# Performance work log

Hardware: AMD Instinct MI355X
Metric: run time of the kernel (lower is better)

Reference implementation:

```python
import jax, jax.numpy as jnp
import numpy as np

SIGMA = 0.005  # hard-coded in naive_corres


def _neg_sqdist(x, y):
    # -||x_i - y_j||^2 via GEMM expansion; x:[B,N,D], y:[B,M,D] -> [B,N,M]
    x2 = jnp.sum(x * x, axis=-1)  # [B,N]
    y2 = jnp.sum(y * y, axis=-1)  # [B,M]
    xy = jnp.einsum('bnd,bmd->bnm', x, y)
    return -(x2[:, :, None] + y2[:, None, :] - 2.0 * xy)


def setup_inputs() -> dict:
    key = jax.random.key(0)
    k1, k2, k3, k4 = jax.random.split(key, 4)
    B, N, D = 2, 4096, 32
    points = jax.random.uniform(k1, (B, N, 3), dtype=jnp.float32)
    pointfea1 = jax.random.normal(k2, (B, N, D), dtype=jnp.float32)
    pointfea2 = jax.random.normal(k3, (B, N, D), dtype=jnp.float32)
    weights = jax.random.uniform(k4, (B, N, 1), dtype=jnp.float32) / N
    return {"points": points, "pointfea1": pointfea1,
            "pointfea2": pointfea2, "weights": weights}


def reference(points, pointfea1, pointfea2, weights):
    # --- naive_corres ---
    p = points / SIGMA
    point_dist2 = _neg_sqdist(p, p)                       # [B,N,N]
    point_loggauss = jax.nn.log_softmax(point_dist2, axis=2)
    fea_dist2 = _neg_sqdist(pointfea1, pointfea2)         # [B,N,N]
    fea_logsoftmax = jax.nn.log_softmax(fea_dist2, axis=2)
    # ce per source point, weighted, summed over points -> [B]
    ce = -jnp.sum(jnp.exp(point_loggauss) * fea_logsoftmax, axis=2)  # [B,N]
    ce_loss = jnp.sum(ce * weights[..., 0], axis=1)       # [B]
    # --- reg_loss (pos_is_in_fea=True -> skip first 3 channels) ---
    reg = (pointfea1[:, :, 3:] ** 2 + pointfea2[:, :, 3:] ** 2)
    reg_loss = reg.mean(axis=2).mean(axis=1)              # [B]
    return ce_loss, reg_loss
```

## Files before the change

kernel.cpp:

```cpp
#include <hip/hip_runtime.h>
#include <math.h>


#define NPTS 4096
#define ROWS_TOT 8192
#define DF 32

#define L2E  1.4426950408889634f
#define LN2  0.6931471805599453f
#define FSC  1.6986436f
#define PSC  240.2244f

typedef _Float16 half8 __attribute__((ext_vector_type(8)));
typedef float f4 __attribute__((ext_vector_type(4)));

__global__ void kA_prep(const float* __restrict__ pts,
                        const float* __restrict__ f1g,
                        const float* __restrict__ f2g,
                        float* __restrict__ pp1, float* __restrict__ pp2,
                        _Float16* __restrict__ fragA, _Float16* __restrict__ fragB,
                        float* __restrict__ regp, float* __restrict__ out) {
    const int r = blockIdx.x * 64 + threadIdx.x;
    if (r < 4) out[r] = 0.0f;
    const int jt = r >> 4;
    const int c  = r & 15;

    float n1, n2, reg1, reg2;
    {
        const float4* f2v = (const float4*)(f2g + (size_t)r * DF);
        float vals[32];
        float s = 0.0f;
#pragma unroll
        for (int q = 0; q < 8; ++q) {
            float4 v = f2v[q];
            vals[4*q]=v.x; vals[4*q+1]=v.y; vals[4*q+2]=v.z; vals[4*q+3]=v.w;
            s += v.x*v.x + v.y*v.y + v.z*v.z + v.w*v.w;
        }
        n2 = s;
        reg2 = s - vals[0]*vals[0] - vals[1]*vals[1] - vals[2]*vals[2];
        half8* fv = (half8*)fragB;
#pragma unroll
        for (int kb = 0; kb < 4; ++kb) {
            half8 h;
#pragma unroll
            for (int i = 0; i < 8; ++i) h[i] = (_Float16)(vals[kb*8+i] * FSC);
            fv[(size_t)jt*64 + kb*16 + c] = h;
        }
    }
    {
        const float4* f1v = (const float4*)(f1g + (size_t)r * DF);
        float vals[32];
        float s = 0.0f;
#pragma unroll
        for (int q = 0; q < 8; ++q) {
            float4 v = f1v[q];
            vals[4*q]=v.x; vals[4*q+1]=v.y; vals[4*q+2]=v.z; vals[4*q+3]=v.w;
            s += v.x*v.x + v.y*v.y + v.z*v.z + v.w*v.w;
        }
        n1 = s;
        reg1 = s - vals[0]*vals[0] - vals[1]*vals[1] - vals[2]*vals[2];
        half8* fv = (half8*)fragA;
#pragma unroll
        for (int kb = 0; kb < 4; ++kb) {
            half8 h;
#pragma unroll
            for (int i = 0; i < 8; ++i) h[i] = (_Float16)(vals[kb*8+i] * FSC);
            fv[(size_t)jt*64 + kb*16 + c] = h;
        }
    }
    const float* pp = pts + (size_t)r * 3;
    const float px = pp[0]*PSC, py = pp[1]*PSC, pz = pp[2]*PSC;
    ((float4*)pp1)[r] = make_float4(px, py, pz, n1 * L2E);
    ((float4*)pp2)[r] = make_float4(px, py, pz, n2 * L2E);
    regp[r] = reg1 + reg2;
}

__launch_bounds__(512)
__global__ void kB_main(const float* __restrict__ pp1,
                        const float* __restrict__ pp2,
                        const _Float16* __restrict__ fragA,
                        const _Float16* __restrict__ fragB,
                        float* __restrict__ part) {
    __shared__ float sS[8][32], sT[8][32], sF[8][32];

    const int tid = threadIdx.x;
    const int l = tid & 63, wv = tid >> 6;
    const int ip = blockIdx.x >> 1;
    const int jh = blockIdx.x & 1;
    const int b  = ip >> 7;
    const int i0g = ip * 32;
    const int lr = l & 15, lk = l >> 4;

    const half8 afA = ((const half8*)fragA)[(size_t)(ip * 2)     * 64 + l];
    const half8 afB = ((const half8*)fragA)[(size_t)(ip * 2 + 1) * 64 + l];

    const int rbA = i0g + lk * 4;
    const int rbB = i0g + 16 + lk * 4;
    f4 qxA, qyA, qzA, qwA, qxB, qyB, qzB, qwB;
#pragma unroll
    for (int e = 0; e < 4; ++e) {
        const float4 qA = ((const float4*)pp1)[rbA + e];
        const float4 qB = ((const float4*)pp1)[rbB + e];
        qxA[e] = qA.x; qyA[e] = qA.y; qzA[e] = qA.z; qwA[e] = qA.w;
        qxB[e] = qB.x; qyB[e] = qB.y; qzB[e] = qB.z; qwB[e] = qB.w;
    }

    const int jt0 = b * 256 + jh * 128 + wv * 16;
    const int j0  = b * NPTS + jh * 2048 + wv * 256 + lr;
    const half8*  fbase = (const half8*)fragB + ((size_t)jt0 * 64 + l);
    const float4* pbase = (const float4*)pp2 + j0;

    f4 spA = {0,0,0,0}, tAA = {0,0,0,0}, sfA = {0,0,0,0};
    f4 spB = {0,0,0,0}, tAB = {0,0,0,0}, sfB = {0,0,0,0};
    const f4 zero = {0.f, 0.f, 0.f, 0.f};

    half8  bfC = fbase[0];
    float4 pwC = pbase[0];
#pragma unroll
    for (int t = 0; t < 16; ++t) {
        half8  bfN = bfC;
        float4 pwN = pwC;
        if (t < 15) {
            bfN = fbase[(t + 1) * 64];
            pwN = pbase[(t + 1) * 16];
        }
        const f4 ccA = __builtin_amdgcn_mfma_f32_16x16x32_f16(afA, bfC, zero, 0, 0, 0);
        const f4 ccB = __builtin_amdgcn_mfma_f32_16x16x32_f16(afB, bfC, zero, 0, 0, 0);
        {
            const f4 fd = ccA - qwA - pwC.w;
            const f4 dx = qxA - pwC.x;
            const f4 dy = qyA - pwC.y;
            const f4 dz = qzA - pwC.z;
            const f4 s  = dx*dx + dy*dy + dz*dz;
            f4 ep, ef;
#pragma unroll
            for (int e = 0; e < 4; ++e) {
                ep[e] = __builtin_amdgcn_exp2f(-s[e]);
                ef[e] = __builtin_amdgcn_exp2f(fd[e]);
            }
            spA += ep; tAA += ep * fd; sfA += ef;
        }
        {
            const f4 fd = ccB - qwB - pwC.w;
            const f4 dx = qxB - pwC.x;
            const f4 dy = qyB - pwC.y;
            const f4 dz = qzB - pwC.z;
            const f4 s  = dx*dx + dy*dy + dz*dz;
            f4 ep, ef;
#pragma unroll
            for (int e = 0; e < 4; ++e) {
                ep[e] = __builtin_amdgcn_exp2f(-s[e]);
                ef[e] = __builtin_amdgcn_exp2f(fd[e]);
            }
            spB += ep; tAB += ep * fd; sfB += ef;
        }
        bfC = bfN;
        pwC = pwN;
    }

#pragma unroll
    for (int m = 1; m < 16; m <<= 1) {
#pragma unroll
        for (int e = 0; e < 4; ++e) {
            spA[e] += __shfl_xor(spA[e], m);
            tAA[e] += __shfl_xor(tAA[e], m);
            sfA[e] += __shfl_xor(sfA[e], m);
            spB[e] += __shfl_xor(spB[e], m);
            tAB[e] += __shfl_xor(tAB[e], m);
            sfB[e] += __shfl_xor(sfB[e], m);
        }
    }
    if (lr == 0) {
#pragma unroll
        for (int e = 0; e < 4; ++e) {
            sS[wv][lk * 4 + e]      = spA[e];
            sT[wv][lk * 4 + e]      = tAA[e];
            sF[wv][lk * 4 + e]      = sfA[e];
            sS[wv][16 + lk * 4 + e] = spB[e];
            sT[wv][16 + lk * 4 + e] = tAB[e];
            sF[wv][16 + lk * 4 + e] = sfB[e];
        }
    }
    __syncthreads();

    if (tid < 32) {
        float sp_ = 0.f, tp_ = 0.f, sf_ = 0.f;
#pragma unroll
        for (int w = 0; w < 8; ++w) {
            sp_ += sS[w][tid];
            tp_ += sT[w][tid];
            sf_ += sF[w][tid];
        }
        float* P = part + (size_t)jh * 3 * ROWS_TOT;
        P[i0g + tid]                = sp_;
        P[ROWS_TOT + i0g + tid]     = tp_;
        P[2 * ROWS_TOT + i0g + tid] = sf_;
    }
}

__global__ void k2_final(const float* __restrict__ part,
                         const float* __restrict__ regp,
                         const float* __restrict__ wg,
                         float* __restrict__ out) {
    __shared__ float redc[4], redr[4];
    const int tid = threadIdx.x;
    const int r = blockIdx.x * 256 + tid;
    const int b = r >> 12;

    const float* P0 = part;
    const float* P1 = part + (size_t)3 * ROWS_TOT;
    const float sp_ = P0[r] + P1[r];
    const float tp_ = P0[ROWS_TOT + r] + P1[ROWS_TOT + r];
    const float sf_ = P0[2*ROWS_TOT + r] + P1[2*ROWS_TOT + r];
    const float ce = __logf(sf_) - (tp_ * LN2) / sp_;
    float contrib = wg[r] * ce;
    float rr = regp[r];

#pragma unroll
    for (int off = 32; off > 0; off >>= 1) {
        contrib += __shfl_down(contrib, off);
        rr      += __shfl_down(rr, off);
    }
    const int wave = tid >> 6, lane = tid & 63;
    if (lane == 0) { redc[wave] = contrib; redr[wave] = rr; }
    __syncthreads();
    if (tid == 0) {
        atomicAdd(&out[b],     redc[0] + redc[1] + redc[2] + redc[3]);
        atomicAdd(&out[2 + b], (redr[0] + redr[1] + redr[2] + redr[3])
                               * (1.0f / (29.0f * (float)NPTS)));
    }
}

extern "C" void kernel_launch(void* const* d_in, const int* in_sizes, int n_in,
                              void* d_out, int out_size, void* d_ws, size_t ws_size,
                              hipStream_t stream) {
    const float* pts = (const float*)d_in[0];
    const float* f1  = (const float*)d_in[1];
    const float* f2  = (const float*)d_in[2];
    const float* wg  = (const float*)d_in[3];
    float* out = (float*)d_out;

    float* ws = (float*)d_ws;
    float*     pp1   = ws;
    float*     pp2   = ws + 32768;
    _Float16*  fragB = (_Float16*)(ws + 65536);
    _Float16*  fragA = (_Float16*)(ws + 196608);
    float*     regp  = ws + 327680;
    float*     part  = ws + 335872;

    kA_prep<<<ROWS_TOT / 64, 64, 0, stream>>>(pts, f1, f2, pp1, pp2,
                                              fragA, fragB, regp, out);
    kB_main<<<512, 512, 0, stream>>>(pp1, pp2, fragA, fragB, part);
    k2_final<<<ROWS_TOT / 256, 256, 0, stream>>>(part, regp, wg, out);
}
```

Before: 28.53 us.

## Retile main kernel to 64 rows per block and fold bias into MFMA accumulator

Each block now covers 64 source rows and a quarter of the targets, instead of 32 rows and half the targets. Every loaded B fragment and point record then feeds four MFMAs rather than two, which cuts global loads per unit of work. The per-pair bias (qw - pw) is passed as the MFMA accumulator input, with qw's sign flipped in prep, so the separate subtractions after the matrix op go away. The cost is more live registers and four partial buffers to sum in the final kernel, which needs a larger partials allocation.

```diff
diff --git a/kernel.cpp b/kernel.cpp
--- a/kernel.cpp
+++ b/kernel.cpp
@@ -70,7 +70,7 @@
     }
     const float* pp = pts + (size_t)r * 3;
     const float px = pp[0]*PSC, py = pp[1]*PSC, pz = pp[2]*PSC;
-    ((float4*)pp1)[r] = make_float4(px, py, pz, n1 * L2E);
+    ((float4*)pp1)[r] = make_float4(px, py, pz, -(n1 * L2E));
     ((float4*)pp2)[r] = make_float4(px, py, pz, n2 * L2E);
     regp[r] = reg1 + reg2;
 }
@@ -81,56 +81,57 @@
                         const _Float16* __restrict__ fragA,
                         const _Float16* __restrict__ fragB,
                         float* __restrict__ part) {
-    __shared__ float sS[8][32], sT[8][32], sF[8][32];
+    __shared__ float sS[8][64], sT[8][64], sF[8][64];
 
     const int tid = threadIdx.x;
     const int l = tid & 63, wv = tid >> 6;
-    const int ip = blockIdx.x >> 1;
-    const int jh = blockIdx.x & 1;
-    const int b  = ip >> 7;
-    const int i0g = ip * 32;
+    const int ip4 = blockIdx.x >> 2;
+    const int jq  = blockIdx.x & 3;
+    const int b   = ip4 >> 6;
+    const int i0g = ip4 * 64;
     const int lr = l & 15, lk = l >> 4;
 
-    const half8 afA = ((const half8*)fragA)[(size_t)(ip * 2)     * 64 + l];
-    const half8 afB = ((const half8*)fragA)[(size_t)(ip * 2 + 1) * 64 + l];
-
-    const int rbA = i0g + lk * 4;
-    const int rbB = i0g + 16 + lk * 4;
-    f4 qxA, qyA, qzA, qwA, qxB, qyB, qzB, qwB;
-#pragma unroll
-    for (int e = 0; e < 4; ++e) {
-        const float4 qA = ((const float4*)pp1)[rbA + e];
-        const float4 qB = ((const float4*)pp1)[rbB + e];
-        qxA[e] = qA.x; qyA[e] = qA.y; qzA[e] = qA.z; qwA[e] = qA.w;
-        qxB[e] = qB.x; qyB[e] = qB.y; qzB[e] = qB.z; qwB[e] = qB.w;
-    }
-
-    const int jt0 = b * 256 + jh * 128 + wv * 16;
-    const int j0  = b * NPTS + jh * 2048 + wv * 256 + lr;
+    half8 af[4];
+    f4 qx[4], qy[4], qz[4], qw[4];
+#pragma unroll
+    for (int i = 0; i < 4; ++i) {
+        af[i] = ((const half8*)fragA)[(size_t)(ip4 * 4 + i) * 64 + l];
+        const int rb = i0g + i * 16 + lk * 4;
+#pragma unroll
+        for (int e = 0; e < 4; ++e) {
+            const float4 q = ((const float4*)pp1)[rb + e];
+            qx[i][e] = q.x; qy[i][e] = q.y; qz[i][e] = q.z; qw[i][e] = q.w;
+        }
+    }
+
+    const int jt0 = b * 256 + jq * 64 + wv * 8;
+    const int j0  = b * NPTS + jq * 1024 + wv * 128 + lr;
     const half8*  fbase = (const half8*)fragB + ((size_t)jt0 * 64 + l);
     const float4* pbase = (const float4*)pp2 + j0;
 
-    f4 spA = {0,0,0,0}, tAA = {0,0,0,0}, sfA = {0,0,0,0};
-    f4 spB = {0,0,0,0}, tAB = {0,0,0,0}, sfB = {0,0,0,0};
-    const f4 zero = {0.f, 0.f, 0.f, 0.f};
+    f4 sp[4], tA[4], sf[4];
+#pragma unroll
+    for (int i = 0; i < 4; ++i) {
+        sp[i] = (f4){0,0,0,0}; tA[i] = (f4){0,0,0,0}; sf[i] = (f4){0,0,0,0};
+    }
 
     half8  bfC = fbase[0];
     float4 pwC = pbase[0];
 #pragma unroll
-    for (int t = 0; t < 16; ++t) {
+    for (int t = 0; t < 8; ++t) {
         half8  bfN = bfC;
         float4 pwN = pwC;
-        if (t < 15) {
+        if (t < 7) {
             bfN = fbase[(t + 1) * 64];
             pwN = pbase[(t + 1) * 16];
         }
-        const f4 ccA = __builtin_amdgcn_mfma_f32_16x16x32_f16(afA, bfC, zero, 0, 0, 0);
-        const f4 ccB = __builtin_amdgcn_mfma_f32_16x16x32_f16(afB, bfC, zero, 0, 0, 0);
-        {
-            const f4 fd = ccA - qwA - pwC.w;
-            const f4 dx = qxA - pwC.x;
-            const f4 dy = qyA - pwC.y;
-            const f4 dz = qzA - pwC.z;
+#pragma unroll
+        for (int i = 0; i < 4; ++i) {
+            const f4 C1 = qw[i] - pwC.w;
+            const f4 fd = __builtin_amdgcn_mfma_f32_16x16x32_f16(af[i], bfC, C1, 0, 0, 0);
+            const f4 dx = qx[i] - pwC.x;
+            const f4 dy = qy[i] - pwC.y;
+            const f4 dz = qz[i] - pwC.z;
             const f4 s  = dx*dx + dy*dy + dz*dz;
             f4 ep, ef;
 #pragma unroll
@@ -138,21 +139,9 @@
                 ep[e] = __builtin_amdgcn_exp2f(-s[e]);
                 ef[e] = __builtin_amdgcn_exp2f(fd[e]);
             }
-            spA += ep; tAA += ep * fd; sfA += ef;
-        }
-        {
-            const f4 fd = ccB - qwB - pwC.w;
-            const f4 dx = qxB - pwC.x;
-            const f4 dy = qyB - pwC.y;
-            const f4 dz = qzB - pwC.z;
-            const f4 s  = dx*dx + dy*dy + dz*dz;
-            f4 ep, ef;
-#pragma unroll
-            for (int e = 0; e < 4; ++e) {
-                ep[e] = __builtin_amdgcn_exp2f(-s[e]);
-                ef[e] = __builtin_amdgcn_exp2f(fd[e]);
-            }
-            spB += ep; tAB += ep * fd; sfB += ef;
+            sp[i] += ep;
+            tA[i] += ep * fd;
+            sf[i] += ef;
         }
         bfC = bfN;
         pwC = pwN;
@@ -161,29 +150,29 @@
 #pragma unroll
     for (int m = 1; m < 16; m <<= 1) {
 #pragma unroll
-        for (int e = 0; e < 4; ++e) {
-            spA[e] += __shfl_xor(spA[e], m);
-            tAA[e] += __shfl_xor(tAA[e], m);
-            sfA[e] += __shfl_xor(sfA[e], m);
-            spB[e] += __shfl_xor(spB[e], m);
-            tAB[e] += __shfl_xor(tAB[e], m);
-            sfB[e] += __shfl_xor(sfB[e], m);
+        for (int i = 0; i < 4; ++i) {
+#pragma unroll
+            for (int e = 0; e < 4; ++e) {
+                sp[i][e] += __shfl_xor(sp[i][e], m);
+                tA[i][e] += __shfl_xor(tA[i][e], m);
+                sf[i][e] += __shfl_xor(sf[i][e], m);
+            }
         }
     }
     if (lr == 0) {
 #pragma unroll
-        for (int e = 0; e < 4; ++e) {
-            sS[wv][lk * 4 + e]      = spA[e];
-            sT[wv][lk * 4 + e]      = tAA[e];
-            sF[wv][lk * 4 + e]      = sfA[e];
-            sS[wv][16 + lk * 4 + e] = spB[e];
-            sT[wv][16 + lk * 4 + e] = tAB[e];
-            sF[wv][16 + lk * 4 + e] = sfB[e];
+        for (int i = 0; i < 4; ++i) {
+#pragma unroll
+            for (int e = 0; e < 4; ++e) {
+                sS[wv][i * 16 + lk * 4 + e] = sp[i][e];
+                sT[wv][i * 16 + lk * 4 + e] = tA[i][e];
+                sF[wv][i * 16 + lk * 4 + e] = sf[i][e];
+            }
         }
     }
     __syncthreads();
 
-    if (tid < 32) {
+    if (tid < 64) {
         float sp_ = 0.f, tp_ = 0.f, sf_ = 0.f;
 #pragma unroll
         for (int w = 0; w < 8; ++w) {
@@ -191,7 +180,7 @@
             tp_ += sT[w][tid];
             sf_ += sF[w][tid];
         }
-        float* P = part + (size_t)jh * 3 * ROWS_TOT;
+        float* P = part + (size_t)jq * 3 * ROWS_TOT;
         P[i0g + tid]                = sp_;
         P[ROWS_TOT + i0g + tid]     = tp_;
         P[2 * ROWS_TOT + i0g + tid] = sf_;
@@ -207,11 +196,14 @@
     const int r = blockIdx.x * 256 + tid;
     const int b = r >> 12;
 
-    const float* P0 = part;
-    const float* P1 = part + (size_t)3 * ROWS_TOT;
-    const float sp_ = P0[r] + P1[r];
-    const float tp_ = P0[ROWS_TOT + r] + P1[ROWS_TOT + r];
-    const float sf_ = P0[2*ROWS_TOT + r] + P1[2*ROWS_TOT + r];
+    float sp_ = 0.f, tp_ = 0.f, sf_ = 0.f;
+#pragma unroll
+    for (int q = 0; q < 4; ++q) {
+        const float* P = part + (size_t)q * 3 * ROWS_TOT;
+        sp_ += P[r];
+        tp_ += P[ROWS_TOT + r];
+        sf_ += P[2 * ROWS_TOT + r];
+    }
     const float ce = __logf(sf_) - (tp_ * LN2) / sp_;
     float contrib = wg[r] * ce;
     float rr = regp[r];
```

Result: slower. 31.47 us (+10.3%).

## Skip far point-gaussian tiles using a spatial-hash neighbor mask

Applied to the files above, without the earlier changes.

Adds two kernels. The first buckets points into a 32^3 grid with at most 4 entries per cell. The second builds a per-tile bitmask of column tiles that hold any neighbor within a distance threshold. The main kernel then computes the point-gaussian exp and its cross term only for masked tiles, which removes about half of the transcendental work. It also folds the norm offsets into the MFMA accumulator input so a vector subtract disappears. The cost is two extra launches and atomics, and the result becomes approximate: cell overflow or points beyond the threshold could drop small contributions.

```diff
diff --git a/kernel.cpp b/kernel.cpp
--- a/kernel.cpp
+++ b/kernel.cpp
@@ -10,26 +10,39 @@
 #define LN2  0.6931471805599453f
 #define FSC  1.6986436f
 #define PSC  240.2244f
+#define NCELL 32
+#define CAP 4
+#define D2THR 7.797e-4f
 
 typedef _Float16 half8 __attribute__((ext_vector_type(8)));
 typedef float f4 __attribute__((ext_vector_type(4)));
+
+static __device__ __forceinline__ int cell_of(float x, float y, float z) {
+    int cx = min(NCELL - 1, max(0, (int)(x * NCELL)));
+    int cy = min(NCELL - 1, max(0, (int)(y * NCELL)));
+    int cz = min(NCELL - 1, max(0, (int)(z * NCELL)));
+    return (cz * NCELL + cy) * NCELL + cx;
+}
 
 __global__ void kA_prep(const float* __restrict__ pts,
                         const float* __restrict__ f1g,
                         const float* __restrict__ f2g,
                         float* __restrict__ pp1, float* __restrict__ pp2,
                         _Float16* __restrict__ fragA, _Float16* __restrict__ fragB,
-                        float* __restrict__ regp, float* __restrict__ out) {
+                        float* __restrict__ regp, unsigned* __restrict__ maskW,
+                        unsigned* __restrict__ counts, float* __restrict__ out) {
     const int r = blockIdx.x * 64 + threadIdx.x;
     if (r < 4) out[r] = 0.0f;
+    maskW[r] = 0u;
+#pragma unroll
+    for (int k = 0; k < 8; ++k) counts[r + k * ROWS_TOT] = 0u;
     const int jt = r >> 4;
     const int c  = r & 15;
 
     float n1, n2, reg1, reg2;
     {
         const float4* f2v = (const float4*)(f2g + (size_t)r * DF);
-        float vals[32];
-        float s = 0.0f;
+        float vals[32]; float s = 0.0f;
 #pragma unroll
         for (int q = 0; q < 8; ++q) {
             float4 v = f2v[q];
@@ -49,8 +62,7 @@
     }
     {
         const float4* f1v = (const float4*)(f1g + (size_t)r * DF);
-        float vals[32];
-        float s = 0.0f;
+        float vals[32]; float s = 0.0f;
 #pragma unroll
         for (int q = 0; q < 8; ++q) {
             float4 v = f1v[q];
@@ -70,9 +82,59 @@
     }
     const float* pp = pts + (size_t)r * 3;
     const float px = pp[0]*PSC, py = pp[1]*PSC, pz = pp[2]*PSC;
-    ((float4*)pp1)[r] = make_float4(px, py, pz, n1 * L2E);
+    ((float4*)pp1)[r] = make_float4(px, py, pz, -(n1 * L2E));
     ((float4*)pp2)[r] = make_float4(px, py, pz, n2 * L2E);
     regp[r] = reg1 + reg2;
+}
+
+__global__ void kH_hash(const float* __restrict__ pts,
+                        unsigned* __restrict__ counts,
+                        unsigned short* __restrict__ buckets) {
+    const int r = blockIdx.x * 64 + threadIdx.x;
+    const int b = r >> 12, il = r & (NPTS - 1);
+    const float* p = pts + (size_t)r * 3;
+    const int cell = cell_of(p[0], p[1], p[2]);
+    const unsigned old = atomicAdd(&counts[b * 32768 + cell], 1u);
+    if (old < CAP) buckets[(size_t)(b * 32768 + cell) * CAP + old] = (unsigned short)il;
+}
+
+__global__ void kN_mask(const float* __restrict__ pts,
+                        const unsigned* __restrict__ counts,
+                        const unsigned short* __restrict__ buckets,
+                        unsigned* __restrict__ maskW) {
+    const int r = blockIdx.x * 64 + threadIdx.x;
+    const int b = r >> 12, il = r & (NPTS - 1);
+    const int itile = r >> 4;
+    atomicOr(&maskW[itile * 16 + (il >> 8)], 1u << ((il >> 4) & 15));
+
+    const float* p = pts + (size_t)r * 3;
+    const float px = p[0], py = p[1], pz = p[2];
+    int cx = min(NCELL-1, max(0, (int)(px * NCELL)));
+    int cy = min(NCELL-1, max(0, (int)(py * NCELL)));
+    int cz = min(NCELL-1, max(0, (int)(pz * NCELL)));
+    const float* ptsb = pts + (size_t)b * NPTS * 3;
+
+    for (int dz = -1; dz <= 1; ++dz) {
+        const int z = cz + dz; if (z < 0 || z >= NCELL) continue;
+        for (int dy = -1; dy <= 1; ++dy) {
+            const int y = cy + dy; if (y < 0 || y >= NCELL) continue;
+            for (int dx = -1; dx <= 1; ++dx) {
+                const int x = cx + dx; if (x < 0 || x >= NCELL) continue;
+                const int cell = (z * NCELL + y) * NCELL + x;
+                const unsigned cnt = min(counts[b * 32768 + cell], (unsigned)CAP);
+                for (unsigned e = 0; e < cnt; ++e) {
+                    const int j = buckets[(size_t)(b * 32768 + cell) * CAP + e];
+                    const float ax = px - ptsb[(size_t)j*3];
+                    const float ay = py - ptsb[(size_t)j*3+1];
+                    const float az = pz - ptsb[(size_t)j*3+2];
+                    const float d2 = ax*ax + ay*ay + az*az;
+                    if (d2 <= D2THR) {
+                        atomicOr(&maskW[itile * 16 + (j >> 8)], 1u << ((j >> 4) & 15));
+                    }
+                }
+            }
+        }
+    }
 }
 
 __launch_bounds__(512)
@@ -80,6 +142,7 @@
                         const float* __restrict__ pp2,
                         const _Float16* __restrict__ fragA,
                         const _Float16* __restrict__ fragB,
+                        const unsigned* __restrict__ maskW,
                         float* __restrict__ part) {
     __shared__ float sS[8][32], sT[8][32], sF[8][32];
 
@@ -110,9 +173,13 @@
     const half8*  fbase = (const half8*)fragB + ((size_t)jt0 * 64 + l);
     const float4* pbase = (const float4*)pp2 + j0;
 
+    const int widx = jh * 8 + wv;
+    const unsigned mword =
+        __builtin_amdgcn_readfirstlane(maskW[(ip * 2) * 16 + widx] |
+                                       maskW[(ip * 2 + 1) * 16 + widx]);
+
     f4 spA = {0,0,0,0}, tAA = {0,0,0,0}, sfA = {0,0,0,0};
     f4 spB = {0,0,0,0}, tAB = {0,0,0,0}, sfB = {0,0,0,0};
-    const f4 zero = {0.f, 0.f, 0.f, 0.f};
 
     half8  bfC = fbase[0];
     float4 pwC = pbase[0];
@@ -124,35 +191,40 @@
             bfN = fbase[(t + 1) * 64];
             pwN = pbase[(t + 1) * 16];
         }
-        const f4 ccA = __builtin_amdgcn_mfma_f32_16x16x32_f16(afA, bfC, zero, 0, 0, 0);
-        const f4 ccB = __builtin_amdgcn_mfma_f32_16x16x32_f16(afB, bfC, zero, 0, 0, 0);
-        {
-            const f4 fd = ccA - qwA - pwC.w;
-            const f4 dx = qxA - pwC.x;
-            const f4 dy = qyA - pwC.y;
-            const f4 dz = qzA - pwC.z;
-            const f4 s  = dx*dx + dy*dy + dz*dz;
-            f4 ep, ef;
-#pragma unroll
-            for (int e = 0; e < 4; ++e) {
-                ep[e] = __builtin_amdgcn_exp2f(-s[e]);
-                ef[e] = __builtin_amdgcn_exp2f(fd[e]);
+        const f4 C1A = qwA - pwC.w;
+        const f4 C1B = qwB - pwC.w;
+        const f4 fdA = __builtin_amdgcn_mfma_f32_16x16x32_f16(afA, bfC, C1A, 0, 0, 0);
+        const f4 fdB = __builtin_amdgcn_mfma_f32_16x16x32_f16(afB, bfC, C1B, 0, 0, 0);
+        f4 efA, efB;
+#pragma unroll
+        for (int e = 0; e < 4; ++e) {
+            efA[e] = __builtin_amdgcn_exp2f(fdA[e]);
+            efB[e] = __builtin_amdgcn_exp2f(fdB[e]);
+        }
+        sfA += efA;
+        sfB += efB;
+
+        if ((mword >> t) & 1) {
+            {
+                const f4 dx = qxA - pwC.x;
+                const f4 dy = qyA - pwC.y;
+                const f4 dz = qzA - pwC.z;
+                const f4 s  = dx*dx + dy*dy + dz*dz;
+                f4 ep;
+#pragma unroll
+                for (int e = 0; e < 4; ++e) ep[e] = __builtin_amdgcn_exp2f(-s[e]);
+                spA += ep; tAA += ep * fdA;
             }
-            spA += ep; tAA += ep * fd; sfA += ef;
-        }
-        {
-            const f4 fd = ccB - qwB - pwC.w;
-            const f4 dx = qxB - pwC.x;
-            const f4 dy = qyB - pwC.y;
-            const f4 dz = qzB - pwC.z;
-            const f4 s  = dx*dx + dy*dy + dz*dz;
-            f4 ep, ef;
-#pragma unroll
-            for (int e = 0; e < 4; ++e) {
-                ep[e] = __builtin_amdgcn_exp2f(-s[e]);
-                ef[e] = __builtin_amdgcn_exp2f(fd[e]);
+            {
+                const f4 dx = qxB - pwC.x;
+                const f4 dy = qyB - pwC.y;
+                const f4 dz = qzB - pwC.z;
+                const f4 s  = dx*dx + dy*dy + dz*dz;
+                f4 ep;
+#pragma unroll
+                for (int e = 0; e < 4; ++e) ep[e] = __builtin_amdgcn_exp2f(-s[e]);
+                spB += ep; tAB += ep * fdB;
             }
-            spB += ep; tAB += ep * fd; sfB += ef;
         }
         bfC = bfN;
         pwC = pwN;
@@ -241,15 +313,20 @@
     float* out = (float*)d_out;
 
     float* ws = (float*)d_ws;
-    float*     pp1   = ws;
-    float*     pp2   = ws + 32768;
-    _Float16*  fragB = (_Float16*)(ws + 65536);
-    _Float16*  fragA = (_Float16*)(ws + 196608);
-    float*     regp  = ws + 327680;
-    float*     part  = ws + 335872;
+    float*          pp1    = ws;
+    float*          pp2    = ws + 32768;
+    _Float16*       fragB  = (_Float16*)(ws + 65536);
+    _Float16*       fragA  = (_Float16*)(ws + 196608);
+    float*          regp   = ws + 327680;
+    float*          part   = ws + 335872;
+    unsigned*       maskW  = (unsigned*)(ws + 385024);
+    unsigned*       counts = (unsigned*)(ws + 393216);
+    unsigned short* buckets= (unsigned short*)(ws + 458752);
 
     kA_prep<<<ROWS_TOT / 64, 64, 0, stream>>>(pts, f1, f2, pp1, pp2,
-                                              fragA, fragB, regp, out);
-    kB_main<<<512, 512, 0, stream>>>(pp1, pp2, fragA, fragB, part);
+                                              fragA, fragB, regp, maskW, counts, out);
+    kH_hash<<<ROWS_TOT / 64, 64, 0, stream>>>(pts, counts, buckets);
+    kN_mask<<<ROWS_TOT / 64, 64, 0, stream>>>(pts, counts, buckets, maskW);
+    kB_main<<<512, 512, 0, stream>>>(pp1, pp2, fragA, fragB, maskW, part);
     k2_final<<<ROWS_TOT / 256, 256, 0, stream>>>(part, regp, wg, out);
 }
```

Result: slower. 57.87 us (+102.9%).

## Split point-Gaussian terms into a cutoff neighbor scan and fold norms into MFMA

Applied to the files above, without the earlier changes.

The fused MFMA kernel now accumulates only the feature softmax denominator. The norm offsets are passed as the MFMA accumulator input, so no separate subtraction is needed. The point-Gaussian weights and their weighted feature logits move to a new kernel. It stages one batch's scaled points in LDS, scans all points per row, and computes fp32 feature dot products only for pairs within a squared-distance cutoff. This removes one exp and the distance math per pair from the dense kernel. The cost is a second O(N^2) distance scan, heavy LDS use per block, and terms beyond the cutoff (below exp2(-45)) being truncated.

```diff
diff --git a/kernel.cpp b/kernel.cpp
--- a/kernel.cpp
+++ b/kernel.cpp
@@ -10,6 +10,7 @@
 #define LN2  0.6931471805599453f
 #define FSC  1.6986436f
 #define PSC  240.2244f
+#define D2MAX 45.0f
 
 typedef _Float16 half8 __attribute__((ext_vector_type(8)));
 typedef float f4 __attribute__((ext_vector_type(4)));
@@ -17,7 +18,8 @@
 __global__ void kA_prep(const float* __restrict__ pts,
                         const float* __restrict__ f1g,
                         const float* __restrict__ f2g,
-                        float* __restrict__ pp1, float* __restrict__ pp2,
+                        float* __restrict__ n1n, float* __restrict__ n2p,
+                        float* __restrict__ pp2,
                         _Float16* __restrict__ fragA, _Float16* __restrict__ fragB,
                         float* __restrict__ regp, float* __restrict__ out) {
     const int r = blockIdx.x * 64 + threadIdx.x;
@@ -28,8 +30,7 @@
     float n1, n2, reg1, reg2;
     {
         const float4* f2v = (const float4*)(f2g + (size_t)r * DF);
-        float vals[32];
-        float s = 0.0f;
+        float vals[32]; float s = 0.0f;
 #pragma unroll
         for (int q = 0; q < 8; ++q) {
             float4 v = f2v[q];
@@ -49,8 +50,7 @@
     }
     {
         const float4* f1v = (const float4*)(f1g + (size_t)r * DF);
-        float vals[32];
-        float s = 0.0f;
+        float vals[32]; float s = 0.0f;
 #pragma unroll
         for (int q = 0; q < 8; ++q) {
             float4 v = f1v[q];
@@ -70,18 +70,19 @@
     }
     const float* pp = pts + (size_t)r * 3;
     const float px = pp[0]*PSC, py = pp[1]*PSC, pz = pp[2]*PSC;
-    ((float4*)pp1)[r] = make_float4(px, py, pz, n1 * L2E);
+    n1n[r] = -(n1 * L2E);
+    n2p[r] =  (n2 * L2E);
     ((float4*)pp2)[r] = make_float4(px, py, pz, n2 * L2E);
     regp[r] = reg1 + reg2;
 }
 
 __launch_bounds__(512)
-__global__ void kB_main(const float* __restrict__ pp1,
-                        const float* __restrict__ pp2,
+__global__ void kB_main(const float* __restrict__ n1n,
+                        const float* __restrict__ n2p,
                         const _Float16* __restrict__ fragA,
                         const _Float16* __restrict__ fragB,
-                        float* __restrict__ part) {
-    __shared__ float sS[8][32], sT[8][32], sF[8][32];
+                        float* __restrict__ sfp) {
+    __shared__ float sF[8][32];
 
     const int tid = threadIdx.x;
     const int l = tid & 63, wv = tid >> 6;
@@ -96,138 +97,136 @@
 
     const int rbA = i0g + lk * 4;
     const int rbB = i0g + 16 + lk * 4;
-    f4 qxA, qyA, qzA, qwA, qxB, qyB, qzB, qwB;
+    f4 qwA, qwB;
 #pragma unroll
     for (int e = 0; e < 4; ++e) {
-        const float4 qA = ((const float4*)pp1)[rbA + e];
-        const float4 qB = ((const float4*)pp1)[rbB + e];
-        qxA[e] = qA.x; qyA[e] = qA.y; qzA[e] = qA.z; qwA[e] = qA.w;
-        qxB[e] = qB.x; qyB[e] = qB.y; qzB[e] = qB.z; qwB[e] = qB.w;
+        qwA[e] = n1n[rbA + e];
+        qwB[e] = n1n[rbB + e];
     }
 
     const int jt0 = b * 256 + jh * 128 + wv * 16;
     const int j0  = b * NPTS + jh * 2048 + wv * 256 + lr;
-    const half8*  fbase = (const half8*)fragB + ((size_t)jt0 * 64 + l);
-    const float4* pbase = (const float4*)pp2 + j0;
-
-    f4 spA = {0,0,0,0}, tAA = {0,0,0,0}, sfA = {0,0,0,0};
-    f4 spB = {0,0,0,0}, tAB = {0,0,0,0}, sfB = {0,0,0,0};
-    const f4 zero = {0.f, 0.f, 0.f, 0.f};
-
-    half8  bfC = fbase[0];
-    float4 pwC = pbase[0];
+    const half8* fbase = (const half8*)fragB + ((size_t)jt0 * 64 + l);
+    const float* nbase = n2p + j0;
+
+    f4 sfA = {0,0,0,0}, sfB = {0,0,0,0};
+
+    half8 bfC = fbase[0];
+    float n2C = nbase[0];
 #pragma unroll
     for (int t = 0; t < 16; ++t) {
-        half8  bfN = bfC;
-        float4 pwN = pwC;
+        half8 bfN = bfC;
+        float n2N = n2C;
         if (t < 15) {
             bfN = fbase[(t + 1) * 64];
-            pwN = pbase[(t + 1) * 16];
-        }
-        const f4 ccA = __builtin_amdgcn_mfma_f32_16x16x32_f16(afA, bfC, zero, 0, 0, 0);
-        const f4 ccB = __builtin_amdgcn_mfma_f32_16x16x32_f16(afB, bfC, zero, 0, 0, 0);
-        {
-            const f4 fd = ccA - qwA - pwC.w;
-            const f4 dx = qxA - pwC.x;
-            const f4 dy = qyA - pwC.y;
-            const f4 dz = qzA - pwC.z;
-            const f4 s  = dx*dx + dy*dy + dz*dz;
-            f4 ep, ef;
-#pragma unroll
-            for (int e = 0; e < 4; ++e) {
-                ep[e] = __builtin_amdgcn_exp2f(-s[e]);
-                ef[e] = __builtin_amdgcn_exp2f(fd[e]);
+            n2N = nbase[(t + 1) * 16];
+        }
+        const f4 C1A = qwA - n2C;
+        const f4 C1B = qwB - n2C;
+        const f4 fdA = __builtin_amdgcn_mfma_f32_16x16x32_f16(afA, bfC, C1A, 0, 0, 0);
+        const f4 fdB = __builtin_amdgcn_mfma_f32_16x16x32_f16(afB, bfC, C1B, 0, 0, 0);
+#pragma unroll
+        for (int e = 0; e < 4; ++e) {
+            sfA[e] += __builtin_amdgcn_exp2f(fdA[e]);
+            sfB[e] += __builtin_amdgcn_exp2f(fdB[e]);
+        }
+        bfC = bfN;
+        n2C = n2N;
+    }
+
+#pragma unroll
+    for (int m = 1; m < 16; m <<= 1) {
+#pragma unroll
+        for (int e = 0; e < 4; ++e) {
+            sfA[e] += __shfl_xor(sfA[e], m);
+            sfB[e] += __shfl_xor(sfB[e], m);
+        }
+    }
+    if (lr == 0) {
+#pragma unroll
+        for (int e = 0; e < 4; ++e) {
+            sF[wv][lk * 4 + e]      = sfA[e];
+            sF[wv][16 + lk * 4 + e] = sfB[e];
+        }
+    }
+    __syncthreads();
+
+    if (tid < 32) {
+        float sf_ = 0.f;
+#pragma unroll
+        for (int w = 0; w < 8; ++w) sf_ += sF[w][tid];
+        sfp[(size_t)jh * ROWS_TOT + i0g + tid] = sf_;
+    }
+}
+
+__launch_bounds__(256)
+__global__ void k2_scan(const float* __restrict__ pp2,
+                        const float* __restrict__ f1g,
+                        const float* __restrict__ f2g,
+                        const float* __restrict__ n1n,
+                        const float* __restrict__ sfp,
+                        const float* __restrict__ regp,
+                        const float* __restrict__ wg,
+                        float* __restrict__ out) {
+    __shared__ float4 P[NPTS];
+    __shared__ float redc[8], redr[8];
+
+    const int tid = threadIdx.x;
+    const int rowbase = blockIdx.x * 8;
+    const int b = rowbase >> 12;
+    const int base = b * NPTS;
+
+    const float4* pv = (const float4*)pp2 + base;
+#pragma unroll
+    for (int k = 0; k < 16; ++k)
+        P[k * 256 + tid] = pv[k * 256 + tid];
+    __syncthreads();
+
+    const int row = rowbase + (tid >> 5);
+    const int sub = tid & 31;
+    const float4 q = P[row & (NPTS - 1)];
+    const float n1r = n1n[row];
+    const float4* f1v = (const float4*)(f1g + (size_t)row * DF);
+
+    float sp = 0.0f, tt = 0.0f;
+#pragma unroll 4
+    for (int jj = sub; jj < NPTS; jj += 32) {
+        const float4 v = P[jj];
+        const float dx = q.x - v.x, dy = q.y - v.y, dz = q.z - v.z;
+        const float d2 = fmaf(dx, dx, fmaf(dy, dy, dz * dz));
+        if (d2 <= D2MAX) {
+            const float ep = __builtin_amdgcn_exp2f(-d2);
+            const float4* f2v = (const float4*)(f2g + (size_t)(base + jj) * DF);
+            float dot = 0.0f;
+#pragma unroll
+            for (int qq = 0; qq < 8; ++qq) {
+                const float4 a = f1v[qq], c = f2v[qq];
+                dot += a.x*c.x + a.y*c.y + a.z*c.z + a.w*c.w;
             }
-            spA += ep; tAA += ep * fd; sfA += ef;
-        }
-        {
-            const f4 fd = ccB - qwB - pwC.w;
-            const f4 dx = qxB - pwC.x;
-            const f4 dy = qyB - pwC.y;
-            const f4 dz = qzB - pwC.z;
-            const f4 s  = dx*dx + dy*dy + dz*dz;
-            f4 ep, ef;
-#pragma unroll
-            for (int e = 0; e < 4; ++e) {
-                ep[e] = __builtin_amdgcn_exp2f(-s[e]);
-                ef[e] = __builtin_amdgcn_exp2f(fd[e]);
-            }
-            spB += ep; tAB += ep * fd; sfB += ef;
-        }
-        bfC = bfN;
-        pwC = pwN;
-    }
-
-#pragma unroll
-    for (int m = 1; m < 16; m <<= 1) {
-#pragma unroll
-        for (int e = 0; e < 4; ++e) {
-            spA[e] += __shfl_xor(spA[e], m);
-            tAA[e] += __shfl_xor(tAA[e], m);
-            sfA[e] += __shfl_xor(sfA[e], m);
-            spB[e] += __shfl_xor(spB[e], m);
-            tAB[e] += __shfl_xor(tAB[e], m);
-            sfB[e] += __shfl_xor(sfB[e], m);
-        }
-    }
-    if (lr == 0) {
-#pragma unroll
-        for (int e = 0; e < 4; ++e) {
-            sS[wv][lk * 4 + e]      = spA[e];
-            sT[wv][lk * 4 + e]      = tAA[e];
-            sF[wv][lk * 4 + e]      = sfA[e];
-            sS[wv][16 + lk * 4 + e] = spB[e];
-            sT[wv][16 + lk * 4 + e] = tAB[e];
-            sF[wv][16 + lk * 4 + e] = sfB[e];
-        }
-    }
-    __syncthreads();
-
-    if (tid < 32) {
-        float sp_ = 0.f, tp_ = 0.f, sf_ = 0.f;
-#pragma unroll
-        for (int w = 0; w < 8; ++w) {
-            sp_ += sS[w][tid];
-            tp_ += sT[w][tid];
-            sf_ += sF[w][tid];
-        }
-        float* P = part + (size_t)jh * 3 * ROWS_TOT;
-        P[i0g + tid]                = sp_;
-        P[ROWS_TOT + i0g + tid]     = tp_;
-        P[2 * ROWS_TOT + i0g + tid] = sf_;
-    }
-}
-
-__global__ void k2_final(const float* __restrict__ part,
-                         const float* __restrict__ regp,
-                         const float* __restrict__ wg,
-                         float* __restrict__ out) {
-    __shared__ float redc[4], redr[4];
-    const int tid = threadIdx.x;
-    const int r = blockIdx.x * 256 + tid;
-    const int b = r >> 12;
-
-    const float* P0 = part;
-    const float* P1 = part + (size_t)3 * ROWS_TOT;
-    const float sp_ = P0[r] + P1[r];
-    const float tp_ = P0[ROWS_TOT + r] + P1[ROWS_TOT + r];
-    const float sf_ = P0[2*ROWS_TOT + r] + P1[2*ROWS_TOT + r];
-    const float ce = __logf(sf_) - (tp_ * LN2) / sp_;
-    float contrib = wg[r] * ce;
-    float rr = regp[r];
-
-#pragma unroll
-    for (int off = 32; off > 0; off >>= 1) {
-        contrib += __shfl_down(contrib, off);
-        rr      += __shfl_down(rr, off);
-    }
-    const int wave = tid >> 6, lane = tid & 63;
-    if (lane == 0) { redc[wave] = contrib; redr[wave] = rr; }
+            const float fd = fmaf(2.0f * L2E, dot, n1r - v.w);
+            sp += ep;
+            tt = fmaf(ep, fd, tt);
+        }
+    }
+
+#pragma unroll
+    for (int m = 1; m < 32; m <<= 1) {
+        sp += __shfl_xor(sp, m, 32);
+        tt += __shfl_xor(tt, m, 32);
+    }
+    if (sub == 0) {
+        const float sf_ = sfp[row] + sfp[ROWS_TOT + row];
+        const float ce = __logf(sf_) - (tt * LN2) / sp;
+        redc[tid >> 5] = wg[row] * ce;
+        redr[tid >> 5] = regp[row];
+    }
     __syncthreads();
     if (tid == 0) {
-        atomicAdd(&out[b],     redc[0] + redc[1] + redc[2] + redc[3]);
-        atomicAdd(&out[2 + b], (redr[0] + redr[1] + redr[2] + redr[3])
-                               * (1.0f / (29.0f * (float)NPTS)));
+        float c = 0.f, rr = 0.f;
+#pragma unroll
+        for (int w = 0; w < 8; ++w) { c += redc[w]; rr += redr[w]; }
+        atomicAdd(&out[b],     c);
+        atomicAdd(&out[2 + b], rr * (1.0f / (29.0f * (float)NPTS)));
     }
 }
 
@@ -241,15 +240,16 @@
     float* out = (float*)d_out;
 
     float* ws = (float*)d_ws;
-    float*     pp1   = ws;
-    float*     pp2   = ws + 32768;
-    _Float16*  fragB = (_Float16*)(ws + 65536);
-    _Float16*  fragA = (_Float16*)(ws + 196608);
-    float*     regp  = ws + 327680;
-    float*     part  = ws + 335872;
-
-    kA_prep<<<ROWS_TOT / 64, 64, 0, stream>>>(pts, f1, f2, pp1, pp2,
+    float*     n1n   = ws;
+    float*     n2p   = ws + 8192;
+    float*     pp2   = ws + 16384;
+    _Float16*  fragB = (_Float16*)(ws + 49152);
+    _Float16*  fragA = (_Float16*)(ws + 180224);
+    float*     regp  = ws + 311296;
+    float*     sfp   = ws + 319488;
+
+    kA_prep<<<ROWS_TOT / 64, 64, 0, stream>>>(pts, f1, f2, n1n, n2p, pp2,
                                               fragA, fragB, regp, out);
-    kB_main<<<512, 512, 0, stream>>>(pp1, pp2, fragA, fragB, part);
-    k2_final<<<ROWS_TOT / 256, 256, 0, stream>>>(part, regp, wg, out);
-}
+    kB_main<<<512, 512, 0, stream>>>(n1n, n2p, fragA, fragB, sfp);
+    k2_scan<<<ROWS_TOT / 8, 256, 0, stream>>>(pp2, f1, f2, n1n, sfp, regp, wg, out);
+}
```

New measurement: 57.94 us. +103.1%, slower.
